# Optimization experiments

Measured on AMD Instinct MI355X. Metric: run time of the kernel, lower is better.

## Reference

```python
import jax, jax.numpy as jnp
import numpy as np

N_NODES = 50000

def _gcn_layer(x, src, dst, W, b, n_nodes):
    # x: [N, F_in]; src/dst: [E+N] (self-loops already appended)
    h = x @ W  # [N, F_out]
    deg = jax.ops.segment_sum(jnp.ones_like(dst, dtype=h.dtype), dst, num_segments=n_nodes)
    dinv = jnp.where(deg > 0, jax.lax.rsqrt(deg), 0.0)  # deg^{-1/2}
    norm = dinv[src] * dinv[dst]  # [E+N]
    msg = h[src] * norm[:, None]  # gather + scale
    out = jax.ops.segment_sum(msg, dst, num_segments=n_nodes)  # scatter-add
    return out + b

def setup_inputs() -> dict:
    key = jax.random.key(0)
    k1, k2, k3, k4 = jax.random.split(key, 4)
    d = 128
    E = 800000
    x = jax.random.normal(k1, (N_NODES, d), dtype=jnp.float32)
    edge_index = jax.random.randint(k2, (2, E), 0, N_NODES, dtype=jnp.int64)
    W1 = jax.random.normal(k3, (d, d), dtype=jnp.float32) / np.sqrt(d)
    b1 = jnp.zeros((d,), dtype=jnp.float32)
    W2 = jax.random.normal(k4, (d, d), dtype=jnp.float32) / np.sqrt(d)
    b2 = jnp.zeros((d,), dtype=jnp.float32)
    return {"x": x, "edge_index": edge_index, "W1": W1, "b1": b1, "W2": W2, "b2": b2}

def reference(x, edge_index, W1, b1, W2, b2):
    n = x.shape[0]
    loops = jnp.arange(n, dtype=edge_index.dtype)
    src = jnp.concatenate([edge_index[0], loops])  # add self-loops
    dst = jnp.concatenate([edge_index[1], loops])
    h = _gcn_layer(x, src, dst, W1, b1, n)
    h = jax.nn.relu(h)
    z = _gcn_layer(h, src, dst, W2, b2, n)
    return z
```

## Files before the change

kernel.cpp:

```cpp
#include <hip/hip_runtime.h>
#include <hip/hip_fp16.h>

#define NF 128
#define KC 64
#define NPART 4

typedef _Float16 half8 __attribute__((ext_vector_type(8)));
typedef float    floatx4 __attribute__((ext_vector_type(4)));

__global__ __launch_bounds__(512) void count2_k(
    const int* __restrict__ dst, int* __restrict__ pcnt, int E, int N, int Ec)
{
    __shared__ int lcnt[12544];
    const int p = blockIdx.x & 3, c = blockIdx.x >> 2;
    const int Np = (N + 3) >> 2;
    const int lo = p * Np, hi = min(lo + Np, N);
    const int sz = hi - lo;
    for (int i = threadIdx.x; i < sz; i += 512) lcnt[i] = 0;
    __syncthreads();

    const int e0 = c * Ec, e1 = min(e0 + Ec, E);
    for (int e = e0 + (int)threadIdx.x * 4; e + 3 < e1; e += 512 * 4) {
        int4 d = *(const int4*)(dst + e);
        if (d.x >= lo && d.x < hi) atomicAdd(&lcnt[d.x - lo], 1);
        if (d.y >= lo && d.y < hi) atomicAdd(&lcnt[d.y - lo], 1);
        if (d.z >= lo && d.z < hi) atomicAdd(&lcnt[d.z - lo], 1);
        if (d.w >= lo && d.w < hi) atomicAdd(&lcnt[d.w - lo], 1);
    }
    int rem0 = e0 + ((e1 - e0) & ~3);
    for (int e = rem0 + (int)threadIdx.x; e < e1; e += 512) {
        int d = dst[e];
        if (d >= lo && d < hi) atomicAdd(&lcnt[d - lo], 1);
    }
    __syncthreads();
    for (int i = threadIdx.x; i < sz; i += 512)
        pcnt[(size_t)c * N + lo + i] = lcnt[i];
}

__global__ __launch_bounds__(256) void pscan2_k(
    int* __restrict__ pcnt, float* __restrict__ dinv,
    int* __restrict__ rowptr, int* __restrict__ blocksum, int n, int N, int nb,
    const float* __restrict__ W1, const float* __restrict__ W2,
    __half* __restrict__ WT1, __half* __restrict__ WT2)
{
    if ((int)blockIdx.x >= nb) {
        int idx = ((int)blockIdx.x - nb) * 256 + threadIdx.x;
        const float* W = (idx < 16384) ? W1 : W2;
        __half* WT     = (idx < 16384) ? WT1 : WT2;
        int j = idx & 16383;
        int nn = j & 127, k = j >> 7;
        WT[nn * NF + k] = __float2half(W[k * NF + nn]);
        return;
    }
    __shared__ int sm[256];
    int tid = threadIdx.x;
    int bin = blockIdx.x * 256 + tid;
    int total = 0;
    if (bin < n) {
        #pragma unroll 4
        for (int c = 0; c < KC; c++) {
            size_t o = (size_t)c * N + bin;
            int v = pcnt[o];
            pcnt[o] = total;
            total += v;
        }
        dinv[bin] = rsqrtf((float)total + 1.0f);
    }
    sm[tid] = total;
    __syncthreads();
    #pragma unroll
    for (int d = 1; d < 256; d <<= 1) {
        int t = (tid >= d) ? sm[tid - d] : 0;
        __syncthreads();
        sm[tid] += t;
        __syncthreads();
    }
    if (bin < n) rowptr[bin] = sm[tid] - total;
    if (tid == 255) blocksum[blockIdx.x] = sm[255];
}

__global__ __launch_bounds__(256) void add_off2(
    int* __restrict__ rowptr, const int* __restrict__ blocksum, int n, int E, int nb)
{
    __shared__ int sm[256];
    int tid = threadIdx.x;
    sm[tid] = (tid < nb && tid < (int)blockIdx.x) ? blocksum[tid] : 0;
    __syncthreads();
    #pragma unroll
    for (int d = 128; d > 0; d >>= 1) {
        if (tid < d) sm[tid] += sm[tid + d];
        __syncthreads();
    }
    int offv = sm[0];
    int i = blockIdx.x * 256 + tid;
    if (i < n) rowptr[i] += offv;
    if (blockIdx.x == 0 && tid == 0) rowptr[n] = E;
}

__global__ __launch_bounds__(512) void fill2_k(
    const int* __restrict__ src, const int* __restrict__ dst,
    const int* __restrict__ rowptr, const int* __restrict__ coff,
    int* __restrict__ csr, int E, int N, int Ec)
{
    __shared__ int lcur[12544];
    const int p = blockIdx.x & 3, c = blockIdx.x >> 2;
    const int Np = (N + 3) >> 2;
    const int lo = p * Np, hi = min(lo + Np, N);
    const int sz = hi - lo;
    for (int i = threadIdx.x; i < sz; i += 512)
        lcur[i] = rowptr[lo + i] + coff[(size_t)c * N + lo + i];
    __syncthreads();

    const int e0 = c * Ec, e1 = min(e0 + Ec, E);
    for (int e = e0 + (int)threadIdx.x * 4; e + 3 < e1; e += 512 * 4) {
        int4 d = *(const int4*)(dst + e);
        int4 s = *(const int4*)(src + e);
        if (d.x >= lo && d.x < hi) csr[atomicAdd(&lcur[d.x - lo], 1)] = s.x;
        if (d.y >= lo && d.y < hi) csr[atomicAdd(&lcur[d.y - lo], 1)] = s.y;
        if (d.z >= lo && d.z < hi) csr[atomicAdd(&lcur[d.z - lo], 1)] = s.z;
        if (d.w >= lo && d.w < hi) csr[atomicAdd(&lcur[d.w - lo], 1)] = s.w;
    }
    int rem0 = e0 + ((e1 - e0) & ~3);
    for (int e = rem0 + (int)threadIdx.x; e < e1; e += 512) {
        int d = dst[e];
        if (d >= lo && d < hi) csr[atomicAdd(&lcur[d - lo], 1)] = src[e];
    }
}


template<bool F32IN>
__device__ __forceinline__ void gemm_body(
    const void* __restrict__ Xv, const __half* __restrict__ WT,
    const float* __restrict__ dinv, __half* __restrict__ out, int M, int bid)
{
    __shared__ __half wlds[128][136];
    const int tid = threadIdx.x;

    {
        int r = tid >> 1;
        int c0 = (tid & 1) * 64;
        const half8* s = (const half8*)(WT + (size_t)r * NF + c0);
        half8* d = (half8*)&wlds[r][c0];
        #pragma unroll
        for (int j = 0; j < 8; j++) d[j] = s[j];
    }
    __syncthreads();

    const int wave = tid >> 6, lane = tid & 63;
    const int quad = lane >> 4, l15 = lane & 15;
    const int rowA = bid * 64 + wave * 16 + l15;
    const int rowc = (rowA < M) ? rowA : (M - 1);

    half8 afr[4];
    if (F32IN) {
        const float* X = (const float*)Xv;
        #pragma unroll
        for (int kc = 0; kc < 4; kc++) {
            const floatx4* p = (const floatx4*)(X + (size_t)rowc * NF + kc * 32 + quad * 8);
            floatx4 u = p[0], v = p[1];
            half8 a;
            a[0] = (_Float16)u[0]; a[1] = (_Float16)u[1];
            a[2] = (_Float16)u[2]; a[3] = (_Float16)u[3];
            a[4] = (_Float16)v[0]; a[5] = (_Float16)v[1];
            a[6] = (_Float16)v[2]; a[7] = (_Float16)v[3];
            afr[kc] = a;
        }
    } else {
        const __half* X = (const __half*)Xv;
        #pragma unroll
        for (int kc = 0; kc < 4; kc++)
            afr[kc] = *(const half8*)(X + (size_t)rowc * NF + kc * 32 + quad * 8);
    }

    floatx4 acc[8];
    #pragma unroll
    for (int ct = 0; ct < 8; ct++) { floatx4 z = {0.f, 0.f, 0.f, 0.f}; acc[ct] = z; }

    #pragma unroll
    for (int kc = 0; kc < 4; kc++) {
        #pragma unroll
        for (int ct = 0; ct < 8; ct++) {
            half8 b = *(const half8*)&wlds[ct * 16 + l15][kc * 32 + quad * 8];
            acc[ct] = __builtin_amdgcn_mfma_f32_16x16x32_f16(afr[kc], b, acc[ct], 0, 0, 0);
        }
    }

    const int orow0 = bid * 64 + wave * 16 + quad * 4;
    #pragma unroll
    for (int r = 0; r < 4; r++) {
        int orow = orow0 + r;
        if (orow < M) {
            float s = dinv[orow];
            #pragma unroll
            for (int ct = 0; ct < 8; ct++)
                out[(size_t)orow * NF + ct * 16 + l15] = __float2half(acc[ct][r] * s);
        }
    }
}

__global__ __launch_bounds__(256) void gemm1_k(
    const float* __restrict__ X, const __half* __restrict__ WT,
    const float* __restrict__ dinv, __half* __restrict__ H, int M)
{
    gemm_body<true>(X, WT, dinv, H, M, blockIdx.x);
}

__global__ __launch_bounds__(256) void gemm2_k(
    const __half* __restrict__ A, const __half* __restrict__ WT,
    const float* __restrict__ dinv, __half* __restrict__ H, int M)
{
    gemm_body<false>(A, WT, dinv, H, M, blockIdx.x);
}


__global__ __launch_bounds__(256) void agg_k(
    const __half2* __restrict__ hs, const int* __restrict__ rowptr,
    const int* __restrict__ csr, const float* __restrict__ dinv,
    const float* __restrict__ bias, __half2* __restrict__ outh,
    float* __restrict__ outf, int n)
{
    int wave = threadIdx.x >> 6;
    int lane = threadIdx.x & 63;
    int node = blockIdx.x * 4 + wave;
    if (node >= n) return;

    const int HS = NF / 2;
    float2 acc = __half22float2(hs[(size_t)node * HS + lane]);

    int base = rowptr[node];
    int cnt  = rowptr[node + 1] - base;

    for (int off = 0; off < cnt; off += 64) {
        int m = min(64, cnt - off);
        int idx = 0;
        if (lane < m) idx = __builtin_nontemporal_load(&csr[base + off + lane]);
        int j = 0;
        for (; j + 15 < m; j += 16) {
            int s[16];
            __half2 v[16];
            #pragma unroll
            for (int t = 0; t < 16; t++) s[t] = __shfl(idx, j + t, 64);
            #pragma unroll
            for (int t = 0; t < 16; t++) v[t] = hs[(size_t)s[t] * HS + lane];
            #pragma unroll
            for (int t = 0; t < 16; t++) {
                float2 f = __half22float2(v[t]);
                acc.x += f.x; acc.y += f.y;
            }
        }
        for (; j < m; j += 8) {
            int s[8];
            __half2 v[8];
            #pragma unroll
            for (int t = 0; t < 8; t++) s[t] = __shfl(idx, min(j + t, m - 1), 64);
            #pragma unroll
            for (int t = 0; t < 8; t++) v[t] = hs[(size_t)s[t] * HS + lane];
            #pragma unroll
            for (int t = 0; t < 8; t++) {
                if (j + t < m) {
                    float2 f = __half22float2(v[t]);
                    acc.x += f.x; acc.y += f.y;
                }
            }
        }
    }

    float s = dinv[node];
    float ox = s * acc.x + bias[2 * lane];
    float oy = s * acc.y + bias[2 * lane + 1];
    if (outh) {
        ox = fmaxf(ox, 0.f); oy = fmaxf(oy, 0.f);
        outh[(size_t)node * HS + lane] = __floats2half2_rn(ox, oy);
    } else {
        ((float2*)(outf + (size_t)node * NF))[lane] = make_float2(ox, oy);
    }
}


extern "C" void kernel_launch(void* const* d_in, const int* in_sizes, int n_in,
                              void* d_out, int out_size, void* d_ws, size_t ws_size,
                              hipStream_t stream) {
    const float* x  = (const float*)d_in[0];
    const int*   ei = (const int*)d_in[1];
    const float* W1 = (const float*)d_in[2];
    const float* b1 = (const float*)d_in[3];
    const float* W2 = (const float*)d_in[4];
    const float* b2 = (const float*)d_in[5];
    float* out = (float*)d_out;

    const int N = in_sizes[0] / NF;
    const int E = in_sizes[1] / 2;
    const int* src = ei;
    const int* dst = ei + E;

    char* ws = (char*)d_ws;
    size_t off = 0;
    auto alloc = [&](size_t bytes) {
        void* p = ws + off;
        off += bytes;
        off = (off + 63) & ~(size_t)63;
        return p;
    };
    int*    pcnt   = (int*)alloc((size_t)KC * N * 4);
    int*    rowptr = (int*)alloc((size_t)(N + 1) * 4);
    int*    csr    = (int*)alloc((size_t)E * 4);
    float*  dinv   = (float*)alloc((size_t)N * 4);
    int*    bsum   = (int*)alloc((size_t)256 * 4);
    __half* WT1    = (__half*)alloc((size_t)NF * NF * 2);
    __half* WT2    = (__half*)alloc((size_t)NF * NF * 2);
    __half* H16    = (__half*)alloc((size_t)N * NF * 2);
    __half* A16    = (__half*)alloc((size_t)N * NF * 2);

    int nb = (N + 255) / 256;
    int Ec = (((E + KC - 1) / KC) + 3) & ~3;
    int gb = (N + 63) / 64;
    int ab = (N + 3) / 4;

    count2_k<<<KC * NPART, 512, 0, stream>>>(dst, pcnt, E, N, Ec);
    pscan2_k<<<nb + 128, 256, 0, stream>>>(pcnt, dinv, rowptr, bsum, N, N, nb,
                                           W1, W2, WT1, WT2);
    add_off2<<<nb, 256, 0, stream>>>(rowptr, bsum, N, E, nb);
    fill2_k<<<KC * NPART, 512, 0, stream>>>(src, dst, rowptr, pcnt, csr, E, N, Ec);
    gemm1_k<<<gb, 256, 0, stream>>>(x, WT1, dinv, H16, N);
    agg_k<<<ab, 256, 0, stream>>>((const __half2*)H16, rowptr, csr, dinv, b1,
                                  (__half2*)A16, nullptr, N);
    gemm2_k<<<gb, 256, 0, stream>>>(A16, WT2, dinv, H16, N);
    agg_k<<<ab, 256, 0, stream>>>((const __half2*)H16, rowptr, csr, dinv, b2,
                                  nullptr, out, N);
}
```

Before: 216.3 us.

## Fuse offset add, CSR fill and first GEMM into one launch; shrink counts

Merges the add_off2, fill2_k and gemm1_k kernels into a single mid_k launch. Some blocks run a 512-thread, 128-row GEMM, and the others compute the block-prefix offsets locally, write a separate rowptr2, and fill the CSR. Per-chunk counts are stored as 16-bit values to halve pcnt traffic. The aggregation kernel now has each half-wave gather a different neighbour's 4-wide half vector and combines the halves with a shuffle. This removes two kernel launches and lets the GEMM overlap with the CSR fill, at the cost of redundant prefix scans per block and a risk of 16-bit count overflow on larger graphs.

```diff
diff --git a/kernel.cpp b/kernel.cpp
--- a/kernel.cpp
+++ b/kernel.cpp
@@ -4,14 +4,17 @@
 #define NF 128
 #define KC 64
 #define NPART 4
+#define NPMAX 12544
 
 typedef _Float16 half8 __attribute__((ext_vector_type(8)));
+typedef _Float16 half4v __attribute__((ext_vector_type(4)));
 typedef float    floatx4 __attribute__((ext_vector_type(4)));
 
 __global__ __launch_bounds__(512) void count2_k(
-    const int* __restrict__ dst, int* __restrict__ pcnt, int E, int N, int Ec)
-{
-    __shared__ int lcnt[12544];
+    const int* __restrict__ dst, unsigned short* __restrict__ pcnt,
+    int E, int N, int Ec)
+{
+    __shared__ int lcnt[NPMAX];
     const int p = blockIdx.x & 3, c = blockIdx.x >> 2;
     const int Np = (N + 3) >> 2;
     const int lo = p * Np, hi = min(lo + Np, N);
@@ -34,11 +37,11 @@
     }
     __syncthreads();
     for (int i = threadIdx.x; i < sz; i += 512)
-        pcnt[(size_t)c * N + lo + i] = lcnt[i];
+        pcnt[(size_t)c * N + lo + i] = (unsigned short)lcnt[i];
 }
 
 __global__ __launch_bounds__(256) void pscan2_k(
-    int* __restrict__ pcnt, float* __restrict__ dinv,
+    unsigned short* __restrict__ pcnt, float* __restrict__ dinv,
     int* __restrict__ rowptr, int* __restrict__ blocksum, int n, int N, int nb,
     const float* __restrict__ W1, const float* __restrict__ W2,
     __half* __restrict__ WT1, __half* __restrict__ WT2)
@@ -61,7 +64,7 @@
         for (int c = 0; c < KC; c++) {
             size_t o = (size_t)c * N + bin;
             int v = pcnt[o];
-            pcnt[o] = total;
+            pcnt[o] = (unsigned short)total;
             total += v;
         }
         dinv[bin] = rsqrtf((float)total + 1.0f);
@@ -79,76 +82,27 @@
     if (tid == 255) blocksum[blockIdx.x] = sm[255];
 }
 
-__global__ __launch_bounds__(256) void add_off2(
-    int* __restrict__ rowptr, const int* __restrict__ blocksum, int n, int E, int nb)
-{
-    __shared__ int sm[256];
-    int tid = threadIdx.x;
-    sm[tid] = (tid < nb && tid < (int)blockIdx.x) ? blocksum[tid] : 0;
-    __syncthreads();
-    #pragma unroll
-    for (int d = 128; d > 0; d >>= 1) {
-        if (tid < d) sm[tid] += sm[tid + d];
-        __syncthreads();
-    }
-    int offv = sm[0];
-    int i = blockIdx.x * 256 + tid;
-    if (i < n) rowptr[i] += offv;
-    if (blockIdx.x == 0 && tid == 0) rowptr[n] = E;
-}
-
-__global__ __launch_bounds__(512) void fill2_k(
-    const int* __restrict__ src, const int* __restrict__ dst,
-    const int* __restrict__ rowptr, const int* __restrict__ coff,
-    int* __restrict__ csr, int E, int N, int Ec)
-{
-    __shared__ int lcur[12544];
-    const int p = blockIdx.x & 3, c = blockIdx.x >> 2;
-    const int Np = (N + 3) >> 2;
-    const int lo = p * Np, hi = min(lo + Np, N);
-    const int sz = hi - lo;
-    for (int i = threadIdx.x; i < sz; i += 512)
-        lcur[i] = rowptr[lo + i] + coff[(size_t)c * N + lo + i];
-    __syncthreads();
-
-    const int e0 = c * Ec, e1 = min(e0 + Ec, E);
-    for (int e = e0 + (int)threadIdx.x * 4; e + 3 < e1; e += 512 * 4) {
-        int4 d = *(const int4*)(dst + e);
-        int4 s = *(const int4*)(src + e);
-        if (d.x >= lo && d.x < hi) csr[atomicAdd(&lcur[d.x - lo], 1)] = s.x;
-        if (d.y >= lo && d.y < hi) csr[atomicAdd(&lcur[d.y - lo], 1)] = s.y;
-        if (d.z >= lo && d.z < hi) csr[atomicAdd(&lcur[d.z - lo], 1)] = s.z;
-        if (d.w >= lo && d.w < hi) csr[atomicAdd(&lcur[d.w - lo], 1)] = s.w;
-    }
-    int rem0 = e0 + ((e1 - e0) & ~3);
-    for (int e = rem0 + (int)threadIdx.x; e < e1; e += 512) {
-        int d = dst[e];
-        if (d >= lo && d < hi) csr[atomicAdd(&lcur[d - lo], 1)] = src[e];
-    }
-}
-
 
 template<bool F32IN>
-__device__ __forceinline__ void gemm_body(
+__device__ __forceinline__ void gemm_body512(
     const void* __restrict__ Xv, const __half* __restrict__ WT,
-    const float* __restrict__ dinv, __half* __restrict__ out, int M, int bid)
-{
-    __shared__ __half wlds[128][136];
+    const float* __restrict__ dinv, __half* __restrict__ out, int M, int bid,
+    __half (*wlds)[136])
+{
     const int tid = threadIdx.x;
-
     {
-        int r = tid >> 1;
-        int c0 = (tid & 1) * 64;
+        int r = tid >> 2;
+        int c0 = (tid & 3) * 32;
         const half8* s = (const half8*)(WT + (size_t)r * NF + c0);
         half8* d = (half8*)&wlds[r][c0];
         #pragma unroll
-        for (int j = 0; j < 8; j++) d[j] = s[j];
+        for (int j = 0; j < 4; j++) d[j] = s[j];
     }
     __syncthreads();
 
     const int wave = tid >> 6, lane = tid & 63;
     const int quad = lane >> 4, l15 = lane & 15;
-    const int rowA = bid * 64 + wave * 16 + l15;
+    const int rowA = bid * 128 + wave * 16 + l15;
     const int rowc = (rowA < M) ? rowA : (M - 1);
 
     half8 afr[4];
@@ -185,7 +139,7 @@
         }
     }
 
-    const int orow0 = bid * 64 + wave * 16 + quad * 4;
+    const int orow0 = bid * 128 + wave * 16 + quad * 4;
     #pragma unroll
     for (int r = 0; r < 4; r++) {
         int orow = orow0 + r;
@@ -198,34 +152,148 @@
     }
 }
 
-__global__ __launch_bounds__(256) void gemm1_k(
+__global__ __launch_bounds__(512) void mid_k(
+    const int* __restrict__ src, const int* __restrict__ dst,
+    const int* __restrict__ rowptr, const unsigned short* __restrict__ coff,
+    const int* __restrict__ blocksum, int* __restrict__ rowptr2,
+    int* __restrict__ csr, int E, int N, int Ec, int nb,
     const float* __restrict__ X, const __half* __restrict__ WT,
-    const float* __restrict__ dinv, __half* __restrict__ H, int M)
-{
-    gemm_body<true>(X, WT, dinv, H, M, blockIdx.x);
+    const float* __restrict__ dinv, __half* __restrict__ H, int GB2)
+{
+    __shared__ __align__(16) char smem[NPMAX * 4 + 1024];
+    const int tid = threadIdx.x;
+    if ((int)blockIdx.x < GB2) {
+        gemm_body512<true>(X, WT, dinv, H, N, blockIdx.x, (__half(*)[136])smem);
+        return;
+    }
+    int* lcur = (int*)smem;
+    int* pref = (int*)(smem + NPMAX * 4);
+
+    const int b = blockIdx.x - GB2;
+    const int p = b & 3, c = b >> 2;
+    const int Np = (N + 3) >> 2;
+    const int lo = p * Np, hi = min(lo + Np, N);
+    const int sz = hi - lo;
+
+    int v = (tid < nb) ? blocksum[tid] : 0;
+    if (tid < 256) pref[tid] = v;
+    __syncthreads();
+    #pragma unroll
+    for (int d = 1; d < 256; d <<= 1) {
+        int t = (tid < 256 && tid >= d) ? pref[tid - d] : 0;
+        __syncthreads();
+        if (tid < 256) pref[tid] += t;
+        __syncthreads();
+    }
+    if (tid < 256) pref[tid] -= v;
+    __syncthreads();
+
+    for (int i = tid; i < sz; i += 512) {
+        int bin = lo + i;
+        int r = rowptr[bin] + pref[bin >> 8] + (int)coff[(size_t)c * N + bin];
+        lcur[i] = r;
+        if (c == 0) rowptr2[bin] = r;
+    }
+    if (c == 0 && p == 0 && tid == 0) rowptr2[N] = E;
+    __syncthreads();
+
+    const int e0 = c * Ec, e1 = min(e0 + Ec, E);
+    for (int e = e0 + tid * 4; e + 3 < e1; e += 512 * 4) {
+        int4 d = *(const int4*)(dst + e);
+        int4 s = *(const int4*)(src + e);
+        if (d.x >= lo && d.x < hi) csr[atomicAdd(&lcur[d.x - lo], 1)] = s.x;
+        if (d.y >= lo && d.y < hi) csr[atomicAdd(&lcur[d.y - lo], 1)] = s.y;
+        if (d.z >= lo && d.z < hi) csr[atomicAdd(&lcur[d.z - lo], 1)] = s.z;
+        if (d.w >= lo && d.w < hi) csr[atomicAdd(&lcur[d.w - lo], 1)] = s.w;
+    }
+    int rem0 = e0 + ((e1 - e0) & ~3);
+    for (int e = rem0 + tid; e < e1; e += 512) {
+        int d = dst[e];
+        if (d >= lo && d < hi) csr[atomicAdd(&lcur[d - lo], 1)] = src[e];
+    }
+}
+
+template<bool F32IN>
+__device__ __forceinline__ void gemm_body256(
+    const void* __restrict__ Xv, const __half* __restrict__ WT,
+    const float* __restrict__ dinv, __half* __restrict__ out, int M, int bid)
+{
+    __shared__ __half wlds[128][136];
+    const int tid = threadIdx.x;
+    {
+        int r = tid >> 1;
+        int c0 = (tid & 1) * 64;
+        const half8* s = (const half8*)(WT + (size_t)r * NF + c0);
+        half8* d = (half8*)&wlds[r][c0];
+        #pragma unroll
+        for (int j = 0; j < 8; j++) d[j] = s[j];
+    }
+    __syncthreads();
+
+    const int wave = tid >> 6, lane = tid & 63;
+    const int quad = lane >> 4, l15 = lane & 15;
+    const int rowA = bid * 64 + wave * 16 + l15;
+    const int rowc = (rowA < M) ? rowA : (M - 1);
+
+    half8 afr[4];
+    const __half* X = (const __half*)Xv;
+    #pragma unroll
+    for (int kc = 0; kc < 4; kc++)
+        afr[kc] = *(const half8*)(X + (size_t)rowc * NF + kc * 32 + quad * 8);
+
+    floatx4 acc[8];
+    #pragma unroll
+    for (int ct = 0; ct < 8; ct++) { floatx4 z = {0.f, 0.f, 0.f, 0.f}; acc[ct] = z; }
+
+    #pragma unroll
+    for (int kc = 0; kc < 4; kc++) {
+        #pragma unroll
+        for (int ct = 0; ct < 8; ct++) {
+            half8 b = *(const half8*)&wlds[ct * 16 + l15][kc * 32 + quad * 8];
+            acc[ct] = __builtin_amdgcn_mfma_f32_16x16x32_f16(afr[kc], b, acc[ct], 0, 0, 0);
+        }
+    }
+
+    const int orow0 = bid * 64 + wave * 16 + quad * 4;
+    #pragma unroll
+    for (int r = 0; r < 4; r++) {
+        int orow = orow0 + r;
+        if (orow < M) {
+            float s = dinv[orow];
+            #pragma unroll
+            for (int ct = 0; ct < 8; ct++)
+                out[(size_t)orow * NF + ct * 16 + l15] = __float2half(acc[ct][r] * s);
+        }
+    }
 }
 
 __global__ __launch_bounds__(256) void gemm2_k(
     const __half* __restrict__ A, const __half* __restrict__ WT,
     const float* __restrict__ dinv, __half* __restrict__ H, int M)
 {
-    gemm_body<false>(A, WT, dinv, H, M, blockIdx.x);
+    gemm_body256<false>(A, WT, dinv, H, M, blockIdx.x);
 }
 
 
 __global__ __launch_bounds__(256) void agg_k(
-    const __half2* __restrict__ hs, const int* __restrict__ rowptr,
+    const __half* __restrict__ hs, const int* __restrict__ rowptr,
     const int* __restrict__ csr, const float* __restrict__ dinv,
-    const float* __restrict__ bias, __half2* __restrict__ outh,
+    const float* __restrict__ bias, __half* __restrict__ outh,
     float* __restrict__ outf, int n)
 {
     int wave = threadIdx.x >> 6;
     int lane = threadIdx.x & 63;
     int node = blockIdx.x * 4 + wave;
     if (node >= n) return;
-
-    const int HS = NF / 2;
-    float2 acc = __half22float2(hs[(size_t)node * HS + lane]);
+    const int eg = lane >> 5, fl = lane & 31;
+
+    const half4v* hs4 = (const half4v*)hs;
+    floatx4 acc = {0.f, 0.f, 0.f, 0.f};
+    if (eg == 0) {
+        half4v s = hs4[(size_t)node * 32 + fl];
+        acc[0] = (float)s[0]; acc[1] = (float)s[1];
+        acc[2] = (float)s[2]; acc[3] = (float)s[3];
+    }
 
     int base = rowptr[node];
     int cnt  = rowptr[node + 1] - base;
@@ -234,45 +302,43 @@
         int m = min(64, cnt - off);
         int idx = 0;
         if (lane < m) idx = __builtin_nontemporal_load(&csr[base + off + lane]);
-        int j = 0;
-        for (; j + 15 < m; j += 16) {
-            int s[16];
-            __half2 v[16];
-            #pragma unroll
-            for (int t = 0; t < 16; t++) s[t] = __shfl(idx, j + t, 64);
-            #pragma unroll
-            for (int t = 0; t < 16; t++) v[t] = hs[(size_t)s[t] * HS + lane];
-            #pragma unroll
-            for (int t = 0; t < 16; t++) {
-                float2 f = __half22float2(v[t]);
-                acc.x += f.x; acc.y += f.y;
-            }
-        }
-        for (; j < m; j += 8) {
+        for (int j = 0; j < m; j += 16) {
             int s[8];
-            __half2 v[8];
-            #pragma unroll
-            for (int t = 0; t < 8; t++) s[t] = __shfl(idx, min(j + t, m - 1), 64);
-            #pragma unroll
-            for (int t = 0; t < 8; t++) v[t] = hs[(size_t)s[t] * HS + lane];
+            half4v v[8];
+            #pragma unroll
+            for (int t = 0; t < 8; t++)
+                s[t] = __shfl(idx, min(j + 2 * t + eg, m - 1), 64);
+            #pragma unroll
+            for (int t = 0; t < 8; t++)
+                v[t] = hs4[(size_t)s[t] * 32 + fl];
             #pragma unroll
             for (int t = 0; t < 8; t++) {
-                if (j + t < m) {
-                    float2 f = __half22float2(v[t]);
-                    acc.x += f.x; acc.y += f.y;
+                if (j + 2 * t + eg < m) {
+                    acc[0] += (float)v[t][0]; acc[1] += (float)v[t][1];
+                    acc[2] += (float)v[t][2]; acc[3] += (float)v[t][3];
                 }
             }
         }
     }
 
-    float s = dinv[node];
-    float ox = s * acc.x + bias[2 * lane];
-    float oy = s * acc.y + bias[2 * lane + 1];
-    if (outh) {
-        ox = fmaxf(ox, 0.f); oy = fmaxf(oy, 0.f);
-        outh[(size_t)node * HS + lane] = __floats2half2_rn(ox, oy);
-    } else {
-        ((float2*)(outf + (size_t)node * NF))[lane] = make_float2(ox, oy);
+    #pragma unroll
+    for (int k = 0; k < 4; k++) acc[k] += __shfl_xor(acc[k], 32, 64);
+
+    if (eg == 0) {
+        float dv = dinv[node];
+        float o0 = dv * acc[0] + bias[fl * 4];
+        float o1 = dv * acc[1] + bias[fl * 4 + 1];
+        float o2 = dv * acc[2] + bias[fl * 4 + 2];
+        float o3 = dv * acc[3] + bias[fl * 4 + 3];
+        if (outh) {
+            half4v h;
+            h[0] = (_Float16)fmaxf(o0, 0.f); h[1] = (_Float16)fmaxf(o1, 0.f);
+            h[2] = (_Float16)fmaxf(o2, 0.f); h[3] = (_Float16)fmaxf(o3, 0.f);
+            *(half4v*)&outh[(size_t)node * NF + fl * 4] = h;
+        } else {
+            floatx4 w = {o0, o1, o2, o3};
+            *(floatx4*)(outf + (size_t)node * NF + fl * 4) = w;
+        }
     }
 }
 
@@ -301,30 +367,30 @@
         off = (off + 63) & ~(size_t)63;
         return p;
     };
-    int*    pcnt   = (int*)alloc((size_t)KC * N * 4);
-    int*    rowptr = (int*)alloc((size_t)(N + 1) * 4);
-    int*    csr    = (int*)alloc((size_t)E * 4);
-    float*  dinv   = (float*)alloc((size_t)N * 4);
-    int*    bsum   = (int*)alloc((size_t)256 * 4);
-    __half* WT1    = (__half*)alloc((size_t)NF * NF * 2);
-    __half* WT2    = (__half*)alloc((size_t)NF * NF * 2);
-    __half* H16    = (__half*)alloc((size_t)N * NF * 2);
-    __half* A16    = (__half*)alloc((size_t)N * NF * 2);
-
-    int nb = (N + 255) / 256;
-    int Ec = (((E + KC - 1) / KC) + 3) & ~3;
-    int gb = (N + 63) / 64;
-    int ab = (N + 3) / 4;
+    unsigned short* pcnt = (unsigned short*)alloc((size_t)KC * N * 2);
+    int*    rowptr  = (int*)alloc((size_t)(N + 1) * 4);
+    int*    rowptr2 = (int*)alloc((size_t)(N + 1) * 4);
+    int*    csr     = (int*)alloc((size_t)E * 4);
+    float*  dinv    = (float*)alloc((size_t)N * 4);
+    int*    bsum    = (int*)alloc((size_t)256 * 4);
+    __half* WT1     = (__half*)alloc((size_t)NF * NF * 2);
+    __half* WT2     = (__half*)alloc((size_t)NF * NF * 2);
+    __half* H16     = (__half*)alloc((size_t)N * NF * 2);
+    __half* A16     = (__half*)alloc((size_t)N * NF * 2);
+
+    int nb  = (N + 255) / 256;
+    int Ec  = (((E + KC - 1) / KC) + 3) & ~3;
+    int GB2 = (N + 127) / 128;
+    int gb  = (N + 63) / 64;
+    int ab  = (N + 3) / 4;
 
     count2_k<<<KC * NPART, 512, 0, stream>>>(dst, pcnt, E, N, Ec);
     pscan2_k<<<nb + 128, 256, 0, stream>>>(pcnt, dinv, rowptr, bsum, N, N, nb,
                                            W1, W2, WT1, WT2);
-    add_off2<<<nb, 256, 0, stream>>>(rowptr, bsum, N, E, nb);
-    fill2_k<<<KC * NPART, 512, 0, stream>>>(src, dst, rowptr, pcnt, csr, E, N, Ec);
-    gemm1_k<<<gb, 256, 0, stream>>>(x, WT1, dinv, H16, N);
-    agg_k<<<ab, 256, 0, stream>>>((const __half2*)H16, rowptr, csr, dinv, b1,
-                                  (__half2*)A16, nullptr, N);
+    mid_k<<<GB2 + KC * NPART, 512, 0, stream>>>(src, dst, rowptr, pcnt, bsum,
+                                                rowptr2, csr, E, N, Ec, nb,
+                                                x, WT1, dinv, H16, GB2);
+    agg_k<<<ab, 256, 0, stream>>>(H16, rowptr2, csr, dinv, b1, A16, nullptr, N);
     gemm2_k<<<gb, 256, 0, stream>>>(A16, WT2, dinv, H16, N);
-    agg_k<<<ab, 256, 0, stream>>>((const __half2*)H16, rowptr, csr, dinv, b2,
-                                  nullptr, out, N);
-}
+    agg_k<<<ab, 256, 0, stream>>>(H16, rowptr2, csr, dinv, b2, nullptr, out, N);
+}
```

Result: faster. 210.3 us (-2.7%).
